# Optimization experiments

Hardware: AMD Instinct MI355X
Metric: run time of the kernel (lower is better)

## Reference

```python
import jax, jax.numpy as jnp
import numpy as np
import math

LAMBDA_INIT = 0.8 - 0.6 * math.exp(-0.3 * 2)  # depth=2


def setup_inputs() -> dict:
    key = jax.random.key(0)
    ks = jax.random.split(key, 10)
    B, T, E, hd = 1, 2048, 1024, 32
    s = 0.02
    return {
        "x": jax.random.normal(ks[0], (B, T, E), jnp.float32),
        "Wq": jax.random.normal(ks[1], (E, E), jnp.float32) * s,
        "Wk": jax.random.normal(ks[2], (E, E), jnp.float32) * s,
        "Wv": jax.random.normal(ks[3], (E, E), jnp.float32) * s,
        "Wo": jax.random.normal(ks[4], (E, E), jnp.float32) * s,
        "lambda_q1": jax.random.normal(ks[5], (hd,), jnp.float32) * 0.1,
        "lambda_k1": jax.random.normal(ks[6], (hd,), jnp.float32) * 0.1,
        "lambda_q2": jax.random.normal(ks[7], (hd,), jnp.float32) * 0.1,
        "lambda_k2": jax.random.normal(ks[8], (hd,), jnp.float32) * 0.1,
        "gamma": jnp.ones((2 * hd,), jnp.float32),
    }


def reference(x, Wq, Wk, Wv, Wo, lambda_q1, lambda_k1, lambda_q2, lambda_k2, gamma):
    B, T, E = x.shape
    hd = gamma.shape[0] // 2          # head_dim
    H = E // (2 * hd)                 # num_heads
    scaling = hd ** -0.5

    # projections (torch Linear: y = x @ W.T)
    q = (x @ Wq.T).reshape(B, T, 2 * H, hd).transpose(0, 2, 1, 3)  # [B,2H,T,hd]
    k = (x @ Wk.T).reshape(B, T, 2 * H, hd).transpose(0, 2, 1, 3)  # [B,2H,T,hd]
    v = (x @ Wv.T).reshape(B, T, H, 2 * hd).transpose(0, 2, 1, 3)  # [B,H,T,2hd]

    # causal mask (offset = 0 since src_len == tgt_len)
    mask = jnp.triu(jnp.full((T, T), -jnp.inf, jnp.float32), k=1)

    attn_weights = jnp.einsum('bhtd,bhsd->bhts', q * scaling, k) + mask
    attn_weights = jax.nn.softmax(attn_weights.astype(jnp.float32), axis=-1).astype(x.dtype)

    lambda_1 = jnp.exp(jnp.sum(lambda_q1 * lambda_k1).astype(jnp.float32))
    lambda_2 = jnp.exp(jnp.sum(lambda_q2 * lambda_k2).astype(jnp.float32))
    lambda_full = (lambda_1 - lambda_2 + LAMBDA_INIT).astype(x.dtype)

    aw = attn_weights.reshape(B, H, 2, T, T)
    diff = aw[:, :, 0] - lambda_full * aw[:, :, 1]          # [B,H,T,T]

    attn = jnp.einsum('bhts,bhsd->bhtd', diff, v)            # [B,H,T,2hd]

    # RMSNorm over last dim (computed in fp32)
    a32 = attn.astype(jnp.float32)
    normed = a32 * jax.lax.rsqrt(jnp.mean(a32 * a32, axis=-1, keepdims=True) + 1e-5)
    attn = gamma * normed.astype(attn.dtype)
    attn = attn * (1 - LAMBDA_INIT)

    attn = attn.transpose(0, 2, 1, 3).reshape(B, T, E)
    return attn @ Wo.T
```

## Files before the change

kernel.cpp:

```cpp
#include <hip/hip_runtime.h>
#include <math.h>

typedef float f32x4 __attribute__((ext_vector_type(4)));
typedef __bf16 bf16x8 __attribute__((ext_vector_type(8)));

#define MFMA16(a, b, c) __builtin_amdgcn_mfma_f32_16x16x32_bf16((a), (b), (c), 0, 0, 0)

__device__ __forceinline__ unsigned short f2bf(float f) {
    union { float f; unsigned u; } v; v.f = f;
    return (unsigned short)((v.u + 0x7fffu + ((v.u >> 16) & 1u)) >> 16);
}
__device__ __forceinline__ unsigned pack2(float a, float b) {
    return (unsigned)f2bf(a) | ((unsigned)f2bf(b) << 16);
}

__global__ __launch_bounds__(256)
void convert_bf16(const float* __restrict__ x,  const float* __restrict__ wq,
                  const float* __restrict__ wk, const float* __restrict__ wv,
                  const float* __restrict__ wo,
                  unsigned short* __restrict__ xb,  unsigned short* __restrict__ wqb,
                  unsigned short* __restrict__ wkb, unsigned short* __restrict__ wvb,
                  unsigned short* __restrict__ wob)
{
    int i = blockIdx.x * 256 + threadIdx.x;
    const float* s; unsigned short* d; int o;
    if (i < 524288)       { s = x;  d = xb;  o = i; }
    else if (i < 786432)  { s = wq; d = wqb; o = i - 524288; }
    else if (i < 1048576) { s = wk; d = wkb; o = i - 786432; }
    else if (i < 1310720) { s = wv; d = wvb; o = i - 1048576; }
    else                  { s = wo; d = wob; o = i - 1310720; }
    float4 v = *reinterpret_cast<const float4*>(s + (size_t)o * 4);
    ushort4 r;
    r.x = f2bf(v.x); r.y = f2bf(v.y); r.z = f2bf(v.z); r.w = f2bf(v.w);
    *reinterpret_cast<ushort4*>(d + (size_t)o * 4) = r;
}

__device__ __forceinline__ void gemm_bf16_body(const unsigned short* __restrict__ A,
                                               const unsigned short* __restrict__ W,
                                               void* __restrict__ Cp, int mode)
{
    __shared__ char Al[128 * 128];
    __shared__ char Bl[64 * 128];

    const int tid = threadIdx.x;
    const int lane = tid & 63, w = tid >> 6;
    const int g = lane >> 4, r15 = lane & 15;
    const int wm = (w >> 1) * 64, wn = (w & 1) * 32;
    const int m0 = blockIdx.y * 128, n0 = blockIdx.x * 64;

    f32x4 acc[4][2] = {};

    for (int k0 = 0; k0 < 1024; k0 += 64) {
        __syncthreads();
#pragma unroll
        for (int p = 0; p < 4; p++) {
            int idx = p * 256 + tid;
            int row = idx >> 3, c8 = idx & 7;
            bf16x8 v = *reinterpret_cast<const bf16x8*>(A + (size_t)(m0 + row) * 1024 + k0 + c8 * 8);
            int byte = (row * 128 + c8 * 16) ^ ((row & 7) << 4);
            *reinterpret_cast<bf16x8*>(Al + byte) = v;
        }
#pragma unroll
        for (int p = 0; p < 2; p++) {
            int idx = p * 256 + tid;
            int row = idx >> 3, c8 = idx & 7;
            bf16x8 v = *reinterpret_cast<const bf16x8*>(W + (size_t)(n0 + row) * 1024 + k0 + c8 * 8);
            int byte = (row * 128 + c8 * 16) ^ ((row & 7) << 4);
            *reinterpret_cast<bf16x8*>(Bl + byte) = v;
        }
        __syncthreads();
#pragma unroll
        for (int c = 0; c < 2; c++) {
            bf16x8 af[4], bfr[2];
#pragma unroll
            for (int m = 0; m < 4; m++) {
                int row = wm + m * 16 + r15;
                int byte = (row * 128 + g * 16 + c * 64) ^ ((row & 7) << 4);
                af[m] = *reinterpret_cast<const bf16x8*>(Al + byte);
            }
#pragma unroll
            for (int n = 0; n < 2; n++) {
                int row = wn + n * 16 + r15;
                int byte = (row * 128 + g * 16 + c * 64) ^ ((row & 7) << 4);
                bfr[n] = *reinterpret_cast<const bf16x8*>(Bl + byte);
            }
#pragma unroll
            for (int m = 0; m < 4; m++)
#pragma unroll
                for (int n = 0; n < 2; n++)
                    acc[m][n] = MFMA16(af[m], bfr[n], acc[m][n]);
        }
    }

    if (mode == 0 || mode == 3) {
        const float cs = (mode == 3) ? 0.25504190132624806f : 1.0f;
        unsigned short* C = (unsigned short*)Cp;
#pragma unroll
        for (int m = 0; m < 4; m++)
#pragma unroll
            for (int n = 0; n < 2; n++)
#pragma unroll
                for (int i = 0; i < 4; i++)
                    C[(size_t)(m0 + wm + m * 16 + g * 4 + i) * 1024 + n0 + wn + n * 16 + r15] =
                        f2bf(acc[m][n][i] * cs);
    } else if (mode == 1) {
        unsigned short* C = (unsigned short*)Cp;
#pragma unroll
        for (int m = 0; m < 4; m++)
#pragma unroll
            for (int n = 0; n < 2; n++) {
                unsigned long long v = (unsigned long long)pack2(acc[m][n][0], acc[m][n][1])
                                     | ((unsigned long long)pack2(acc[m][n][2], acc[m][n][3]) << 32);
                *reinterpret_cast<unsigned long long*>(
                    C + (size_t)(n0 + wn + n * 16 + r15) * 2048 + m0 + wm + m * 16 + g * 4) = v;
            }
    } else {
        float* C = (float*)Cp;
#pragma unroll
        for (int m = 0; m < 4; m++)
#pragma unroll
            for (int n = 0; n < 2; n++)
#pragma unroll
                for (int i = 0; i < 4; i++)
                    C[(size_t)(m0 + wm + m * 16 + g * 4 + i) * 1024 + n0 + wn + n * 16 + r15] =
                        acc[m][n][i];
    }
}

__global__ __launch_bounds__(256)
void gemm_qkv_bf16(const unsigned short* __restrict__ xb, const unsigned short* __restrict__ wqb,
                   const unsigned short* __restrict__ wkb, const unsigned short* __restrict__ wvb,
                   unsigned short* __restrict__ Qb, unsigned short* __restrict__ Kb,
                   unsigned short* __restrict__ Vtb)
{
    int z = blockIdx.z;
    const unsigned short* W = (z == 0) ? wqb : (z == 1) ? wkb : wvb;
    void* C = (z == 0) ? (void*)Qb : (z == 1) ? (void*)Kb : (void*)Vtb;
    gemm_bf16_body(xb, W, C, (z == 2) ? 1 : (z == 0 ? 3 : 0));
}

__global__ __launch_bounds__(256)
void gemm_out_bf16(const unsigned short* __restrict__ Nb, const unsigned short* __restrict__ wob,
                   float* __restrict__ out)
{
    gemm_bf16_body(Nb, wob, out, 2);
}

__global__ __launch_bounds__(128)
void attn_mfma2(const unsigned short* __restrict__ Qb, const unsigned short* __restrict__ Kb,
                const unsigned short* __restrict__ Vtb, unsigned short* __restrict__ Nb,
                const float* __restrict__ lq1, const float* __restrict__ lk1,
                const float* __restrict__ lq2, const float* __restrict__ lk2,
                const float* __restrict__ gamma)
{
    __shared__ char Kl[64 * 128];
    __shared__ char Vl[64 * 128];
    __shared__ char Pl[2][32 * 128];

    const int tid = threadIdx.x, lane = tid & 63, w = tid >> 6;
    const int g = lane >> 4, r15 = lane & 15;
    const int u = blockIdx.x >> 4, h = blockIdx.x & 15;
    const int qb = (u < 32) ? u : 95 - u;
    const int q0 = qb * 32;
    const int row_g = q0 + w * 16 + r15;
    const int prow  = w * 16 + r15;

    float s1 = 0.f, s2 = 0.f;
#pragma unroll
    for (int i = 0; i < 32; i++) { s1 += lq1[i] * lk1[i]; s2 += lq2[i] * lk2[i]; }
    const float LI = 0.4707130183435841f;
    const float lam = expf(s1) - expf(s2) + LI;

    bf16x8 qf0 = *reinterpret_cast<const bf16x8*>(Qb + (size_t)row_g * 1024 + h * 64 + g * 8);
    bf16x8 qf1 = *reinterpret_cast<const bf16x8*>(Qb + (size_t)row_g * 1024 + h * 64 + 32 + g * 8);

    f32x4 oacc[2][4] = {};
    float m_u[2] = {-INFINITY, -INFINITY};
    float l_l[2] = {0.f, 0.f};

    const int nkb = (qb + 2) >> 1;
    for (int kb = 0; kb < nkb; kb++) {
        const int j0 = kb * 64;
        __syncthreads();
#pragma unroll
        for (int p = 0; p < 4; p++) {
            int idx = p * 128 + tid;
            int row = idx >> 3, c8 = idx & 7;
            bf16x8 v = *reinterpret_cast<const bf16x8*>(Kb + (size_t)(j0 + row) * 1024 + h * 64 + c8 * 8);
            int byte = (row * 128 + c8 * 16) ^ ((row & 7) << 4);
            *reinterpret_cast<bf16x8*>(Kl + byte) = v;
        }
#pragma unroll
        for (int p = 0; p < 4; p++) {
            int idx = p * 128 + tid;
            int row = idx >> 3, c8 = idx & 7;
            bf16x8 v = *reinterpret_cast<const bf16x8*>(Vtb + (size_t)(h * 64 + row) * 2048 + j0 + c8 * 8);
            int byte = (row * 128 + c8 * 16) ^ ((row & 7) << 4);
            *reinterpret_cast<bf16x8*>(Vl + byte) = v;
        }
        __syncthreads();

        f32x4 sc0[4] = {}, sc1[4] = {};
#pragma unroll
        for (int m = 0; m < 4; m++) {
            int row = m * 16 + r15;
            int b0 = (row * 128 + g * 16) ^ ((row & 7) << 4);
            int b1 = (row * 128 + g * 16 + 64) ^ ((row & 7) << 4);
            bf16x8 a0 = *reinterpret_cast<const bf16x8*>(Kl + b0);
            bf16x8 a1 = *reinterpret_cast<const bf16x8*>(Kl + b1);
            sc0[m] = MFMA16(a0, qf0, sc0[m]);
            sc1[m] = MFMA16(a1, qf1, sc1[m]);
        }

        const bool diag = (kb == nkb - 1);
#pragma unroll
        for (int s = 0; s < 2; s++) {
            f32x4* sc = s ? sc1 : sc0;
            float sv[4][4];
            float mxl = -INFINITY;
            if (diag) {
#pragma unroll
                for (int m = 0; m < 4; m++)
#pragma unroll
                    for (int i = 0; i < 4; i++) {
                        float xv = ((j0 + m * 16 + g * 4 + i) <= row_g) ? sc[m][i] : -INFINITY;
                        sv[m][i] = xv;
                        mxl = fmaxf(mxl, xv);
                    }
            } else {
#pragma unroll
                for (int m = 0; m < 4; m++)
#pragma unroll
                    for (int i = 0; i < 4; i++) {
                        sv[m][i] = sc[m][i];
                        mxl = fmaxf(mxl, sc[m][i]);
                    }
            }
            if (__any(mxl > m_u[s] + 8.0f)) {
                float wm = mxl;
                wm = fmaxf(wm, __shfl_xor(wm, 1));
                wm = fmaxf(wm, __shfl_xor(wm, 2));
                wm = fmaxf(wm, __shfl_xor(wm, 4));
                wm = fmaxf(wm, __shfl_xor(wm, 8));
                wm = fmaxf(wm, __shfl_xor(wm, 16));
                wm = fmaxf(wm, __shfl_xor(wm, 32));
                const float corr = exp2f(m_u[s] - wm);
                m_u[s] = wm;
                l_l[s] *= corr;
#pragma unroll
                for (int n = 0; n < 4; n++)
#pragma unroll
                    for (int i = 0; i < 4; i++) oacc[s][n][i] *= corr;
            }
            float sum = 0.f;
#pragma unroll
            for (int m = 0; m < 4; m++) {
                float p0 = exp2f(sv[m][0] - m_u[s]);
                float p1 = exp2f(sv[m][1] - m_u[s]);
                float p2 = exp2f(sv[m][2] - m_u[s]);
                float p3 = exp2f(sv[m][3] - m_u[s]);
                sum += (p0 + p1) + (p2 + p3);
                unsigned long long pv = (unsigned long long)pack2(p0, p1)
                                      | ((unsigned long long)pack2(p2, p3) << 32);
                int byte = (prow * 128 + m * 32 + g * 8) ^ ((prow & 7) << 4);
                *reinterpret_cast<unsigned long long*>(Pl[s] + byte) = pv;
            }
            l_l[s] += sum;
        }

#pragma unroll
        for (int c = 0; c < 2; c++) {
            int pb = (prow * 128 + g * 16 + c * 64) ^ ((prow & 7) << 4);
            bf16x8 p0 = *reinterpret_cast<const bf16x8*>(Pl[0] + pb);
            bf16x8 p1 = *reinterpret_cast<const bf16x8*>(Pl[1] + pb);
#pragma unroll
            for (int n = 0; n < 4; n++) {
                int vrow = n * 16 + r15;
                int vb = (vrow * 128 + g * 16 + c * 64) ^ ((vrow & 7) << 4);
                bf16x8 vf = *reinterpret_cast<const bf16x8*>(Vl + vb);
                oacc[0][n] = MFMA16(p0, vf, oacc[0][n]);
                oacc[1][n] = MFMA16(p1, vf, oacc[1][n]);
            }
        }
    }

    float l0 = l_l[0];
    l0 += __shfl_xor(l0, 16); l0 += __shfl_xor(l0, 32);
    float l1 = l_l[1];
    l1 += __shfl_xor(l1, 16); l1 += __shfl_xor(l1, 32);
    const float r1 = 1.f / l0;
    const float r2 = lam / l1;
    float i1[4], i2[4];
#pragma unroll
    for (int i = 0; i < 4; i++) {
        i1[i] = __shfl(r1, g * 4 + i);
        i2[i] = __shfl(r2, g * 4 + i);
    }
    float o[4][4], ss[4] = {0.f, 0.f, 0.f, 0.f};
#pragma unroll
    for (int n = 0; n < 4; n++)
#pragma unroll
        for (int i = 0; i < 4; i++) {
            float v = oacc[0][n][i] * i1[i] - oacc[1][n][i] * i2[i];
            o[n][i] = v;
            ss[i] = fmaf(v, v, ss[i]);
        }
#pragma unroll
    for (int i = 0; i < 4; i++) {
        ss[i] += __shfl_xor(ss[i], 1);
        ss[i] += __shfl_xor(ss[i], 2);
        ss[i] += __shfl_xor(ss[i], 4);
        ss[i] += __shfl_xor(ss[i], 8);
    }
    const float post = 1.f - LI;
    float gm4[4];
#pragma unroll
    for (int n = 0; n < 4; n++) gm4[n] = gamma[n * 16 + r15];
#pragma unroll
    for (int i = 0; i < 4; i++) {
        const float rs = rsqrtf(ss[i] * 0.015625f + 1e-5f);
#pragma unroll
        for (int n = 0; n < 4; n++) {
            Nb[(size_t)(q0 + w * 16 + g * 4 + i) * 1024 + h * 64 + n * 16 + r15] =
                f2bf(o[n][i] * rs * gm4[n] * post);
        }
    }
}

extern "C" void kernel_launch(void* const* d_in, const int* in_sizes, int n_in,
                              void* d_out, int out_size, void* d_ws, size_t ws_size,
                              hipStream_t stream)
{
    const float* x   = (const float*)d_in[0];
    const float* Wq  = (const float*)d_in[1];
    const float* Wk  = (const float*)d_in[2];
    const float* Wv  = (const float*)d_in[3];
    const float* Wo  = (const float*)d_in[4];
    const float* lq1 = (const float*)d_in[5];
    const float* lk1 = (const float*)d_in[6];
    const float* lq2 = (const float*)d_in[7];
    const float* lk2 = (const float*)d_in[8];
    const float* gm  = (const float*)d_in[9];
    float* out = (float*)d_out;

    unsigned short* ws  = (unsigned short*)d_ws;
    unsigned short* xb  = ws;
    unsigned short* wqb = xb  + 2097152;
    unsigned short* wkb = wqb + 1048576;
    unsigned short* wvb = wkb + 1048576;
    unsigned short* wob = wvb + 1048576;
    unsigned short* Qb  = wob + 1048576;
    unsigned short* Kb  = Qb  + 2097152;
    unsigned short* Vtb = Kb  + 2097152;
    unsigned short* Nb  = Vtb + 2097152;

    convert_bf16<<<6144, 256, 0, stream>>>(x, Wq, Wk, Wv, Wo, xb, wqb, wkb, wvb, wob);
    gemm_qkv_bf16<<<dim3(16, 16, 3), 256, 0, stream>>>(xb, wqb, wkb, wvb, Qb, Kb, Vtb);
    attn_mfma2<<<1024, 128, 0, stream>>>(Qb, Kb, Vtb, Nb, lq1, lk1, lq2, lk2, gm);
    gemm_out_bf16<<<dim3(16, 16), 256, 0, stream>>>(Nb, wob, out);
}
```

Before: 192.0 us.

## Register-prefetch GEMM tiles and use single-wave attention blocks loading K/V directly

The GEMM body now prefetches the next K-slice of A and W into registers while the current tile sits in shared memory, so global load latency overlaps with MFMA work. The attention kernel is restructured into 64-thread blocks that each handle 16 query rows. K and V fragments are loaded straight from global memory into registers instead of being staged through shared memory, which removes the block-level barriers. The grid doubles to 2048 blocks, scheduled longest-first, to improve load balance. The cost is that K/V reuse across waves is lost, so global and L2 traffic grows, and register pressure rises.

```diff
diff --git a/kernel.cpp b/kernel.cpp
--- a/kernel.cpp
+++ b/kernel.cpp
@@ -49,6 +49,20 @@
     const int m0 = blockIdx.y * 128, n0 = blockIdx.x * 64;
 
     f32x4 acc[4][2] = {};
+    bf16x8 ra[4], rb[2];
+
+#pragma unroll
+    for (int p = 0; p < 4; p++) {
+        int idx = p * 256 + tid;
+        int row = idx >> 3, c8 = idx & 7;
+        ra[p] = *reinterpret_cast<const bf16x8*>(A + (size_t)(m0 + row) * 1024 + c8 * 8);
+    }
+#pragma unroll
+    for (int p = 0; p < 2; p++) {
+        int idx = p * 256 + tid;
+        int row = idx >> 3, c8 = idx & 7;
+        rb[p] = *reinterpret_cast<const bf16x8*>(W + (size_t)(n0 + row) * 1024 + c8 * 8);
+    }
 
     for (int k0 = 0; k0 < 1024; k0 += 64) {
         __syncthreads();
@@ -56,17 +70,29 @@
         for (int p = 0; p < 4; p++) {
             int idx = p * 256 + tid;
             int row = idx >> 3, c8 = idx & 7;
-            bf16x8 v = *reinterpret_cast<const bf16x8*>(A + (size_t)(m0 + row) * 1024 + k0 + c8 * 8);
             int byte = (row * 128 + c8 * 16) ^ ((row & 7) << 4);
-            *reinterpret_cast<bf16x8*>(Al + byte) = v;
+            *reinterpret_cast<bf16x8*>(Al + byte) = ra[p];
         }
 #pragma unroll
         for (int p = 0; p < 2; p++) {
             int idx = p * 256 + tid;
             int row = idx >> 3, c8 = idx & 7;
-            bf16x8 v = *reinterpret_cast<const bf16x8*>(W + (size_t)(n0 + row) * 1024 + k0 + c8 * 8);
             int byte = (row * 128 + c8 * 16) ^ ((row & 7) << 4);
-            *reinterpret_cast<bf16x8*>(Bl + byte) = v;
+            *reinterpret_cast<bf16x8*>(Bl + byte) = rb[p];
+        }
+        if (k0 + 64 < 1024) {
+#pragma unroll
+            for (int p = 0; p < 4; p++) {
+                int idx = p * 256 + tid;
+                int row = idx >> 3, c8 = idx & 7;
+                ra[p] = *reinterpret_cast<const bf16x8*>(A + (size_t)(m0 + row) * 1024 + k0 + 64 + c8 * 8);
+            }
+#pragma unroll
+            for (int p = 0; p < 2; p++) {
+                int idx = p * 256 + tid;
+                int row = idx >> 3, c8 = idx & 7;
+                rb[p] = *reinterpret_cast<const bf16x8*>(W + (size_t)(n0 + row) * 1024 + k0 + 64 + c8 * 8);
+            }
         }
         __syncthreads();
 #pragma unroll
@@ -146,24 +172,21 @@
     gemm_bf16_body(Nb, wob, out, 2);
 }
 
-__global__ __launch_bounds__(128)
-void attn_mfma2(const unsigned short* __restrict__ Qb, const unsigned short* __restrict__ Kb,
+__global__ __launch_bounds__(64, 3)
+void attn_mfma3(const unsigned short* __restrict__ Qb, const unsigned short* __restrict__ Kb,
                 const unsigned short* __restrict__ Vtb, unsigned short* __restrict__ Nb,
                 const float* __restrict__ lq1, const float* __restrict__ lk1,
                 const float* __restrict__ lq2, const float* __restrict__ lk2,
                 const float* __restrict__ gamma)
 {
-    __shared__ char Kl[64 * 128];
-    __shared__ char Vl[64 * 128];
-    __shared__ char Pl[2][32 * 128];
-
-    const int tid = threadIdx.x, lane = tid & 63, w = tid >> 6;
+    __shared__ char Pl[2][16 * 128];
+
+    const int lane = threadIdx.x;
     const int g = lane >> 4, r15 = lane & 15;
     const int u = blockIdx.x >> 4, h = blockIdx.x & 15;
-    const int qb = (u < 32) ? u : 95 - u;
-    const int q0 = qb * 32;
-    const int row_g = q0 + w * 16 + r15;
-    const int prow  = w * 16 + r15;
+    const int qb = 127 - u;
+    const int q0 = qb * 16;
+    const int row_g = q0 + r15;
 
     float s1 = 0.f, s2 = 0.f;
 #pragma unroll
@@ -174,42 +197,37 @@
     bf16x8 qf0 = *reinterpret_cast<const bf16x8*>(Qb + (size_t)row_g * 1024 + h * 64 + g * 8);
     bf16x8 qf1 = *reinterpret_cast<const bf16x8*>(Qb + (size_t)row_g * 1024 + h * 64 + 32 + g * 8);
 
+    const unsigned short* Kh = Kb + h * 64;
+    const unsigned short* Vh = Vtb + (size_t)(h * 64) * 2048;
+
     f32x4 oacc[2][4] = {};
     float m_u[2] = {-INFINITY, -INFINITY};
     float l_l[2] = {0.f, 0.f};
 
-    const int nkb = (qb + 2) >> 1;
+    const int nkb = (q0 + 79) >> 6;
     for (int kb = 0; kb < nkb; kb++) {
         const int j0 = kb * 64;
-        __syncthreads();
-#pragma unroll
-        for (int p = 0; p < 4; p++) {
-            int idx = p * 128 + tid;
-            int row = idx >> 3, c8 = idx & 7;
-            bf16x8 v = *reinterpret_cast<const bf16x8*>(Kb + (size_t)(j0 + row) * 1024 + h * 64 + c8 * 8);
-            int byte = (row * 128 + c8 * 16) ^ ((row & 7) << 4);
-            *reinterpret_cast<bf16x8*>(Kl + byte) = v;
-        }
-#pragma unroll
-        for (int p = 0; p < 4; p++) {
-            int idx = p * 128 + tid;
-            int row = idx >> 3, c8 = idx & 7;
-            bf16x8 v = *reinterpret_cast<const bf16x8*>(Vtb + (size_t)(h * 64 + row) * 2048 + j0 + c8 * 8);
-            int byte = (row * 128 + c8 * 16) ^ ((row & 7) << 4);
-            *reinterpret_cast<bf16x8*>(Vl + byte) = v;
-        }
-        __syncthreads();
+
+        bf16x8 ka0[4], ka1[4];
+#pragma unroll
+        for (int m = 0; m < 4; m++) {
+            const unsigned short* kp = Kh + (size_t)(j0 + m * 16 + r15) * 1024 + g * 8;
+            ka0[m] = *reinterpret_cast<const bf16x8*>(kp);
+            ka1[m] = *reinterpret_cast<const bf16x8*>(kp + 32);
+        }
+        bf16x8 vf[4][2];
+#pragma unroll
+        for (int n = 0; n < 4; n++) {
+            const unsigned short* vp = Vh + (size_t)(n * 16 + r15) * 2048 + j0 + g * 8;
+            vf[n][0] = *reinterpret_cast<const bf16x8*>(vp);
+            vf[n][1] = *reinterpret_cast<const bf16x8*>(vp + 32);
+        }
 
         f32x4 sc0[4] = {}, sc1[4] = {};
 #pragma unroll
         for (int m = 0; m < 4; m++) {
-            int row = m * 16 + r15;
-            int b0 = (row * 128 + g * 16) ^ ((row & 7) << 4);
-            int b1 = (row * 128 + g * 16 + 64) ^ ((row & 7) << 4);
-            bf16x8 a0 = *reinterpret_cast<const bf16x8*>(Kl + b0);
-            bf16x8 a1 = *reinterpret_cast<const bf16x8*>(Kl + b1);
-            sc0[m] = MFMA16(a0, qf0, sc0[m]);
-            sc1[m] = MFMA16(a1, qf1, sc1[m]);
+            sc0[m] = MFMA16(ka0[m], qf0, sc0[m]);
+            sc1[m] = MFMA16(ka1[m], qf1, sc1[m]);
         }
 
         const bool diag = (kb == nkb - 1);
@@ -262,7 +280,7 @@
                 sum += (p0 + p1) + (p2 + p3);
                 unsigned long long pv = (unsigned long long)pack2(p0, p1)
                                       | ((unsigned long long)pack2(p2, p3) << 32);
-                int byte = (prow * 128 + m * 32 + g * 8) ^ ((prow & 7) << 4);
+                int byte = (r15 * 128 + m * 32 + g * 8) ^ ((r15 & 7) << 4);
                 *reinterpret_cast<unsigned long long*>(Pl[s] + byte) = pv;
             }
             l_l[s] += sum;
@@ -270,16 +288,13 @@
 
 #pragma unroll
         for (int c = 0; c < 2; c++) {
-            int pb = (prow * 128 + g * 16 + c * 64) ^ ((prow & 7) << 4);
+            int pb = (r15 * 128 + g * 16 + c * 64) ^ ((r15 & 7) << 4);
             bf16x8 p0 = *reinterpret_cast<const bf16x8*>(Pl[0] + pb);
             bf16x8 p1 = *reinterpret_cast<const bf16x8*>(Pl[1] + pb);
 #pragma unroll
             for (int n = 0; n < 4; n++) {
-                int vrow = n * 16 + r15;
-                int vb = (vrow * 128 + g * 16 + c * 64) ^ ((vrow & 7) << 4);
-                bf16x8 vf = *reinterpret_cast<const bf16x8*>(Vl + vb);
-                oacc[0][n] = MFMA16(p0, vf, oacc[0][n]);
-                oacc[1][n] = MFMA16(p1, vf, oacc[1][n]);
+                oacc[0][n] = MFMA16(p0, vf[n][c], oacc[0][n]);
+                oacc[1][n] = MFMA16(p1, vf[n][c], oacc[1][n]);
             }
         }
     }
@@ -321,7 +336,7 @@
         const float rs = rsqrtf(ss[i] * 0.015625f + 1e-5f);
 #pragma unroll
         for (int n = 0; n < 4; n++) {
-            Nb[(size_t)(q0 + w * 16 + g * 4 + i) * 1024 + h * 64 + n * 16 + r15] =
+            Nb[(size_t)(q0 + g * 4 + i) * 1024 + h * 64 + n * 16 + r15] =
                 f2bf(o[n][i] * rs * gm4[n] * post);
         }
     }
@@ -356,6 +371,6 @@
 
     convert_bf16<<<6144, 256, 0, stream>>>(x, Wq, Wk, Wv, Wo, xb, wqb, wkb, wvb, wob);
     gemm_qkv_bf16<<<dim3(16, 16, 3), 256, 0, stream>>>(xb, wqb, wkb, wvb, Qb, Kb, Vtb);
-    attn_mfma2<<<1024, 128, 0, stream>>>(Qb, Kb, Vtb, Nb, lq1, lk1, lq2, lk2, gm);
+    attn_mfma3<<<2048, 64, 0, stream>>>(Qb, Kb, Vtb, Nb, lq1, lk1, lq2, lk2, gm);
     gemm_out_bf16<<<dim3(16, 16), 256, 0, stream>>>(Nb, wob, out);
 }
```

New measurement: 197.3 us. +2.7%, slower.
